# Optimization experiments

Hardware: AMD Instinct MI355X
Metric: run time of the kernel (lower is better)

The kernel has to match this reference:

```python
import jax, jax.numpy as jnp
import numpy as np

IN_FEATURES = 4096
OUT_FEATURES = 16384
I8_MAX = 127.0
I8_MIN = -128.0


def setup_inputs() -> dict:
    key = jax.random.key(0)
    kx, kw, kb = jax.random.split(key, 3)
    x = jax.random.normal(kx, (2, 4096, IN_FEATURES), dtype=jnp.float32)
    # Original nn.Linear weight [out, in]; QuantLinear stores W.T as int8 [in, out]
    w = jax.random.normal(kw, (OUT_FEATURES, IN_FEATURES), dtype=jnp.float32) * 0.02
    wt = w.T  # [in, out]
    # per-output-channel scale: max_abs over axis=0 of W.T, divided by int8 max
    weight_scale = jnp.max(jnp.abs(wt), axis=0) / I8_MAX  # [out]
    weight_q = jnp.clip(jnp.round(wt / weight_scale[None, :]), I8_MIN, I8_MAX).astype(jnp.int8)
    bias = jax.random.normal(kb, (OUT_FEATURES,), dtype=jnp.float32) * 0.02
    return {"x": x, "weight_q": weight_q, "weight_scale": weight_scale, "bias": bias}


def reference(x, weight_q, weight_scale, bias):
    # flatten leading dims -> [M, in]
    x2 = x.reshape(-1, x.shape[-1])
    # dynamic per-token activation quantization (input_scale is None in module)
    x_scale = jnp.max(jnp.abs(x2), axis=-1, keepdims=True) / I8_MAX  # [M, 1]
    x_scale = jnp.maximum(x_scale, jnp.float32(1e-12))
    x_q = jnp.clip(jnp.round(x2 / x_scale), I8_MIN, I8_MAX)  # integer-valued f32
    # scaled int8 GEMM + dequant (accumulate in f32; values exactly representable)
    acc = jnp.matmul(x_q, weight_q.astype(jnp.float32))  # [M, out]
    out = acc * x_scale * weight_scale[None, :] + bias[None, :]
    return out.reshape(*x.shape[:-1], weight_q.shape[1])
```

## Files before the change

### kernel.cpp

```cpp
#include <hip/hip_runtime.h>
#include <cstdint>
#include <cstddef>

#define IN_F  4096
#define OUT_F 16384
#define NROWS 8192
#define NKT   64

#define NTBLK 16384
#define NQBLK 1024

typedef __attribute__((ext_vector_type(4)))  int int32x4;
typedef __attribute__((ext_vector_type(16))) int int32x16;

__device__ __forceinline__ void gload_lds16(const void* g, void* s) {
    __builtin_amdgcn_global_load_lds((const __attribute__((address_space(1))) void*)g,
                                     (__attribute__((address_space(3))) void*)s,
                                     16, 0, 0);
}


__global__ __launch_bounds__(256) void prep_kernel(const int* __restrict__ w,
                                                   const float* __restrict__ x,
                                                   uint8_t* __restrict__ wtS,
                                                   uint8_t* __restrict__ xqS,
                                                   float* __restrict__ xs) {
    __shared__ uint32_t tl[64][17];
    const int b = blockIdx.x;
    const int t = threadIdx.x;

    if (b < NTBLK) {
        const int nb = (b & 255) * 64;
        const int kt = b >> 8;
        const int r  = t >> 4;
        const int c  = t & 15;

        const int* src = w + (size_t)(kt * 64 + 4 * r) * OUT_F + nb + 4 * c;
        uint32_t wk[4];
#pragma unroll
        for (int i = 0; i < 4; ++i) {
            int4 u = *reinterpret_cast<const int4*>(src + (size_t)i * OUT_F);
            wk[i] = (uint32_t)(u.x & 255) | ((uint32_t)(u.y & 255) << 8)
                  | ((uint32_t)(u.z & 255) << 16) | ((uint32_t)u.w << 24);
        }
#pragma unroll
        for (int j = 0; j < 4; ++j) {
            uint32_t v = ((wk[0] >> (8 * j)) & 255)
                       | (((wk[1] >> (8 * j)) & 255) << 8)
                       | (((wk[2] >> (8 * j)) & 255) << 16)
                       | (((wk[3] >> (8 * j)) & 255) << 24);
            tl[4 * c + j][r] = v;
        }
        __syncthreads();

        const int n  = t >> 2;
        const int qq = t & 3;
        uint4 o;
        o.x = tl[n][4 * qq];
        o.y = tl[n][4 * qq + 1];
        o.z = tl[n][4 * qq + 2];
        o.w = tl[n][4 * qq + 3];
        const int ntile = nb >> 8;
        const int colg  = (nb & 255) + n;
        *reinterpret_cast<uint4*>(wtS + (((size_t)ntile * NKT + kt) * 4 + qq) * 4096 + colg * 16) = o;
    } else {
        const int qb = b - NTBLK;
        const int wv = t >> 6, l = t & 63;
        const int half = l >> 5, lh = l & 31;
        const int m = qb * 8 + wv * 2 + half;
        const float* xr = x + (size_t)m * IN_F;

        float am = 0.0f;
#pragma unroll 8
        for (int jj = 0; jj < 32; ++jj) {
            float4 v = reinterpret_cast<const float4*>(xr)[jj * 32 + lh];
            am = fmaxf(am, fmaxf(fmaxf(fabsf(v.x), fabsf(v.y)),
                                 fmaxf(fabsf(v.z), fabsf(v.w))));
        }
#pragma unroll
        for (int off = 16; off; off >>= 1) am = fmaxf(am, __shfl_xor(am, off));

        const float scale = fmaxf(am / 127.0f, 1e-12f);
        if (lh == 0) xs[m] = scale;

        const int mtile = m >> 8, mrow = m & 255;
        uint8_t* ob = xqS + (size_t)mtile * (NKT * 16384) + (size_t)mrow * 16;
#pragma unroll
        for (int j = 0; j < 8; ++j) {
            const int k0 = lh * 128 + j * 16;
            const float4* vp = reinterpret_cast<const float4*>(xr + k0);
            uint4 pk;
            uint32_t* pp = reinterpret_cast<uint32_t*>(&pk);
#pragma unroll
            for (int q = 0; q < 4; ++q) {
                float4 v = vp[q];
                float r0 = fminf(127.f, fmaxf(-128.f, rintf(v.x / scale)));
                float r1 = fminf(127.f, fmaxf(-128.f, rintf(v.y / scale)));
                float r2 = fminf(127.f, fmaxf(-128.f, rintf(v.z / scale)));
                float r3 = fminf(127.f, fmaxf(-128.f, rintf(v.w / scale)));
                pp[q] = ((uint32_t)((int)r0 & 255)) | ((uint32_t)((int)r1 & 255) << 8)
                      | ((uint32_t)((int)r2 & 255) << 16) | ((uint32_t)((int)r3 & 255) << 24);
            }
            const int ktk = k0 >> 6;
            const int c   = (k0 >> 4) & 3;
            *reinterpret_cast<uint4*>(ob + ((size_t)ktk * 4 + c) * 4096) = pk;
        }
    }
}

__global__ __launch_bounds__(512, 2) void gemm_kernel(const uint8_t* __restrict__ xqS,
                                                      const uint8_t* __restrict__ wtS,
                                                      const float* __restrict__ xs,
                                                      const float* __restrict__ wsc,
                                                      const float* __restrict__ bias,
                                                      float* __restrict__ out) {
    extern __shared__ uint8_t lds[];
    uint8_t* ldsA = lds;
    uint8_t* ldsB = lds + 65536;

    const int t    = threadIdx.x;
    const int lane = t & 63;
    const int wid  = t >> 6;
    const int wm   = wid >> 2, wn = wid & 3;

    const int xcd = blockIdx.x & 7;
    const int i   = blockIdx.x >> 3;
    const int mt  = xcd * 4 + (i & 3);
    const int nt  = i >> 2;

    const uint8_t* aBase = xqS + (size_t)mt * (NKT * 16384);
    const uint8_t* bBase = wtS + (size_t)nt * (NKT * 16384);
    const int t16  = t * 16;
    const int wofs = wid * 1024;

    const int aRd0 = (lane >> 5) * 4096 + wm * 2048 + (lane & 31) * 16;
    const int bRd0 = (lane >> 5) * 4096 + wn * 1024 + (lane & 31) * 16;

    int32x16 acc[4][2] = {};
    int32x4 af0[4], bf0[2], af1[4], bf1[2];

#pragma unroll
    for (int tt = 0; tt < 3; ++tt)
#pragma unroll
        for (int L = 0; L < 2; ++L) {
            gload_lds16(aBase + tt * 16384 + L * 8192 + t16, ldsA + tt * 16384 + L * 8192 + wofs);
            gload_lds16(bBase + tt * 16384 + L * 8192 + t16, ldsB + tt * 16384 + L * 8192 + wofs);
        }
    asm volatile("s_waitcnt vmcnt(8)" ::: "memory");
    __builtin_amdgcn_s_barrier();
    __builtin_amdgcn_sched_barrier(0);

#pragma unroll
    for (int mr = 0; mr < 4; ++mr)
        af0[mr] = *reinterpret_cast<const int32x4*>(ldsA + aRd0 + mr * 512);
#pragma unroll
    for (int nr = 0; nr < 2; ++nr)
        bf0[nr] = *reinterpret_cast<const int32x4*>(ldsB + bRd0 + nr * 512);

    for (int kt = 0; kt < NKT; ++kt) {
        const int q  = (kt & 3) * 16384;
        const int q1 = ((kt + 1) & 3) * 16384;
        const int q3 = ((kt + 3) & 3) * 16384;

#pragma unroll
        for (int mr = 0; mr < 4; ++mr)
            af1[mr] = *reinterpret_cast<const int32x4*>(ldsA + q + 8192 + aRd0 + mr * 512);
#pragma unroll
        for (int nr = 0; nr < 2; ++nr)
            bf1[nr] = *reinterpret_cast<const int32x4*>(ldsB + q + 8192 + bRd0 + nr * 512);

        if (kt < NKT - 3) {
            const size_t src3 = (size_t)(kt + 3) * 16384;
#pragma unroll
            for (int L = 0; L < 2; ++L) {
                gload_lds16(aBase + src3 + L * 8192 + t16, ldsA + q3 + L * 8192 + wofs);
                gload_lds16(bBase + src3 + L * 8192 + t16, ldsB + q3 + L * 8192 + wofs);
            }
        }

        __builtin_amdgcn_s_setprio(1);
#pragma unroll
        for (int mr = 0; mr < 4; ++mr)
#pragma unroll
            for (int nr = 0; nr < 2; ++nr)
                acc[mr][nr] = __builtin_amdgcn_mfma_i32_32x32x32_i8(af0[mr], bf0[nr], acc[mr][nr], 0, 0, 0);
        __builtin_amdgcn_s_setprio(0);

        if (kt < NKT - 1) {
            asm volatile("s_waitcnt lgkmcnt(0)" ::: "memory");
            if (kt < NKT - 3)       asm volatile("s_waitcnt vmcnt(8)" ::: "memory");
            else if (kt == NKT - 3) asm volatile("s_waitcnt vmcnt(4)" ::: "memory");
            else                    asm volatile("s_waitcnt vmcnt(0)" ::: "memory");
            __builtin_amdgcn_s_barrier();
            __builtin_amdgcn_sched_barrier(0);

#pragma unroll
            for (int mr = 0; mr < 4; ++mr)
                af0[mr] = *reinterpret_cast<const int32x4*>(ldsA + q1 + aRd0 + mr * 512);
#pragma unroll
            for (int nr = 0; nr < 2; ++nr)
                bf0[nr] = *reinterpret_cast<const int32x4*>(ldsB + q1 + bRd0 + nr * 512);
        }

        __builtin_amdgcn_s_setprio(1);
#pragma unroll
        for (int mr = 0; mr < 4; ++mr)
#pragma unroll
            for (int nr = 0; nr < 2; ++nr)
                acc[mr][nr] = __builtin_amdgcn_mfma_i32_32x32x32_i8(af1[mr], bf1[nr], acc[mr][nr], 0, 0, 0);
        __builtin_amdgcn_s_setprio(0);
    }

    const int row0 = mt * 256 + wm * 128;
    const int col0 = nt * 256 + wn * 64;
#pragma unroll
    for (int mr = 0; mr < 4; ++mr) {
        const int rbase = row0 + mr * 32 + 4 * (lane >> 5);
        float xsv[16];
#pragma unroll
        for (int g = 0; g < 16; ++g)
            xsv[g] = xs[rbase + (g & 3) + 8 * (g >> 2)];
#pragma unroll
        for (int nr = 0; nr < 2; ++nr) {
            const int n = col0 + nr * 32 + (lane & 31);
            const float ws_n = wsc[n];
            const float b_n  = bias[n];
#pragma unroll
            for (int g = 0; g < 16; ++g) {
                const int m = rbase + (g & 3) + 8 * (g >> 2);
                out[(size_t)m * OUT_F + n] = (float)acc[mr][nr][g] * xsv[g] * ws_n + b_n;
            }
        }
    }
}

extern "C" void kernel_launch(void* const* d_in, const int* in_sizes, int n_in,
                              void* d_out, int out_size, void* d_ws, size_t ws_size,
                              hipStream_t stream) {
    const float* x    = (const float*)d_in[0];
    const int*   wq   = (const int*)d_in[1];
    const float* wsc  = (const float*)d_in[2];
    const float* bias = (const float*)d_in[3];
    float* out = (float*)d_out;

    uint8_t* ws  = (uint8_t*)d_ws;
    uint8_t* wtS = ws;
    uint8_t* xqS = ws + (size_t)IN_F * OUT_F;
    float*   xs  = (float*)(ws + (size_t)IN_F * OUT_F + (size_t)NROWS * IN_F);

    (void)hipFuncSetAttribute((const void*)gemm_kernel,
                              hipFuncAttributeMaxDynamicSharedMemorySize, 131072);

    prep_kernel<<<NTBLK + NQBLK, 256, 0, stream>>>(wq, x, wtS, xqS, xs);
    gemm_kernel<<<(NROWS / 256) * (OUT_F / 256), 512, 131072, stream>>>(xqS, wtS, xs, wsc, bias, out);
}
```

Before: 675.4 us.

## Switch GEMM mainloop to double-buffered 2-K-tile stages with half the barriers

Replaces the 4-slot ring of single K-tiles, with prefetch distance 3, by a two-slot double buffer where each stage holds two K-tiles (four 8 KB sub-chunks). The loop body now runs four register-double-buffered MFMA groups per barrier, halving the number of workgroup barriers and waitcnts. The cost is a shorter prefetch distance (one stage ahead) and a full vmcnt(0) wait each stage, so global-load latency is hidden less deeply.

```diff
diff --git a/kernel.cpp b/kernel.cpp
--- a/kernel.cpp
+++ b/kernel.cpp
@@ -6,6 +6,7 @@
 #define OUT_F 16384
 #define NROWS 8192
 #define NKT   64
+#define NKT2  32
 
 #define NTBLK 16384
 #define NQBLK 1024
@@ -139,76 +140,64 @@
     int32x16 acc[4][2] = {};
     int32x4 af0[4], bf0[2], af1[4], bf1[2];
 
-#pragma unroll
-    for (int tt = 0; tt < 3; ++tt)
-#pragma unroll
-        for (int L = 0; L < 2; ++L) {
-            gload_lds16(aBase + tt * 16384 + L * 8192 + t16, ldsA + tt * 16384 + L * 8192 + wofs);
-            gload_lds16(bBase + tt * 16384 + L * 8192 + t16, ldsB + tt * 16384 + L * 8192 + wofs);
-        }
-    asm volatile("s_waitcnt vmcnt(8)" ::: "memory");
+#define RD_F(AF, BF, OFS)                                                             \
+    {                                                                                 \
+        _Pragma("unroll")                                                             \
+        for (int mr = 0; mr < 4; ++mr)                                                \
+            AF[mr] = *reinterpret_cast<const int32x4*>(ldsA + (OFS) + aRd0 + mr * 512); \
+        _Pragma("unroll")                                                             \
+        for (int nr = 0; nr < 2; ++nr)                                                \
+            BF[nr] = *reinterpret_cast<const int32x4*>(ldsB + (OFS) + bRd0 + nr * 512); \
+    }
+#define MFMA_F(AF, BF)                                                                \
+    {                                                                                 \
+        __builtin_amdgcn_s_setprio(1);                                                \
+        _Pragma("unroll")                                                             \
+        for (int mr = 0; mr < 4; ++mr)                                                \
+            _Pragma("unroll")                                                         \
+            for (int nr = 0; nr < 2; ++nr)                                            \
+                acc[mr][nr] = __builtin_amdgcn_mfma_i32_32x32x32_i8(AF[mr], BF[nr], acc[mr][nr], 0, 0, 0); \
+        __builtin_amdgcn_s_setprio(0);                                                \
+    }
+
+#pragma unroll
+    for (int p = 0; p < 4; ++p) {
+        gload_lds16(aBase + p * 8192 + t16, ldsA + p * 8192 + wofs);
+        gload_lds16(bBase + p * 8192 + t16, ldsB + p * 8192 + wofs);
+    }
+    asm volatile("s_waitcnt vmcnt(0)" ::: "memory");
     __builtin_amdgcn_s_barrier();
     __builtin_amdgcn_sched_barrier(0);
-
-#pragma unroll
-    for (int mr = 0; mr < 4; ++mr)
-        af0[mr] = *reinterpret_cast<const int32x4*>(ldsA + aRd0 + mr * 512);
-#pragma unroll
-    for (int nr = 0; nr < 2; ++nr)
-        bf0[nr] = *reinterpret_cast<const int32x4*>(ldsB + bRd0 + nr * 512);
-
-    for (int kt = 0; kt < NKT; ++kt) {
-        const int q  = (kt & 3) * 16384;
-        const int q1 = ((kt + 1) & 3) * 16384;
-        const int q3 = ((kt + 3) & 3) * 16384;
-
-#pragma unroll
-        for (int mr = 0; mr < 4; ++mr)
-            af1[mr] = *reinterpret_cast<const int32x4*>(ldsA + q + 8192 + aRd0 + mr * 512);
-#pragma unroll
-        for (int nr = 0; nr < 2; ++nr)
-            bf1[nr] = *reinterpret_cast<const int32x4*>(ldsB + q + 8192 + bRd0 + nr * 512);
-
-        if (kt < NKT - 3) {
-            const size_t src3 = (size_t)(kt + 3) * 16384;
-#pragma unroll
-            for (int L = 0; L < 2; ++L) {
-                gload_lds16(aBase + src3 + L * 8192 + t16, ldsA + q3 + L * 8192 + wofs);
-                gload_lds16(bBase + src3 + L * 8192 + t16, ldsB + q3 + L * 8192 + wofs);
+    RD_F(af0, bf0, 0)
+
+    for (int kt2 = 0; kt2 < NKT2; ++kt2) {
+        const int qb = (kt2 & 1) * 32768;
+        const int qn = ((kt2 + 1) & 1) * 32768;
+
+        if (kt2 < NKT2 - 1) {
+            const size_t srcn = (size_t)(kt2 + 1) * 32768;
+#pragma unroll
+            for (int p = 0; p < 4; ++p) {
+                gload_lds16(aBase + srcn + p * 8192 + t16, ldsA + qn + p * 8192 + wofs);
+                gload_lds16(bBase + srcn + p * 8192 + t16, ldsB + qn + p * 8192 + wofs);
             }
         }
 
-        __builtin_amdgcn_s_setprio(1);
-#pragma unroll
-        for (int mr = 0; mr < 4; ++mr)
-#pragma unroll
-            for (int nr = 0; nr < 2; ++nr)
-                acc[mr][nr] = __builtin_amdgcn_mfma_i32_32x32x32_i8(af0[mr], bf0[nr], acc[mr][nr], 0, 0, 0);
-        __builtin_amdgcn_s_setprio(0);
-
-        if (kt < NKT - 1) {
+        RD_F(af1, bf1, qb + 8192)
+        MFMA_F(af0, bf0)
+        RD_F(af0, bf0, qb + 16384)
+        MFMA_F(af1, bf1)
+        RD_F(af1, bf1, qb + 24576)
+        MFMA_F(af0, bf0)
+
+        if (kt2 < NKT2 - 1) {
             asm volatile("s_waitcnt lgkmcnt(0)" ::: "memory");
-            if (kt < NKT - 3)       asm volatile("s_waitcnt vmcnt(8)" ::: "memory");
-            else if (kt == NKT - 3) asm volatile("s_waitcnt vmcnt(4)" ::: "memory");
-            else                    asm volatile("s_waitcnt vmcnt(0)" ::: "memory");
+            asm volatile("s_waitcnt vmcnt(0)" ::: "memory");
             __builtin_amdgcn_s_barrier();
             __builtin_amdgcn_sched_barrier(0);
-
-#pragma unroll
-            for (int mr = 0; mr < 4; ++mr)
-                af0[mr] = *reinterpret_cast<const int32x4*>(ldsA + q1 + aRd0 + mr * 512);
-#pragma unroll
-            for (int nr = 0; nr < 2; ++nr)
-                bf0[nr] = *reinterpret_cast<const int32x4*>(ldsB + q1 + bRd0 + nr * 512);
-        }
-
-        __builtin_amdgcn_s_setprio(1);
-#pragma unroll
-        for (int mr = 0; mr < 4; ++mr)
-#pragma unroll
-            for (int nr = 0; nr < 2; ++nr)
-                acc[mr][nr] = __builtin_amdgcn_mfma_i32_32x32x32_i8(af1[mr], bf1[nr], acc[mr][nr], 0, 0, 0);
-        __builtin_amdgcn_s_setprio(0);
+            RD_F(af0, bf0, qn)
+        }
+        MFMA_F(af1, bf1)
     }
 
     const int row0 = mt * 256 + wm * 128;
```

Measured after the change: 703.7 us. +4.2%, slower.
